# Performance work log

Measured on AMD Instinct MI355X. Metric: run time of the kernel, lower is better.

## Reference

```python
import jax, jax.numpy as jnp
import numpy as np

EMB_DIM = 2048
N_HEADS = 32
N_KV_HEADS = 8
HEAD_DIM = EMB_DIM // N_HEADS  # 64
N_REP = N_HEADS // N_KV_HEADS  # 4
B = 1
T = 2048


def setup_inputs() -> dict:
    key = jax.random.key(0)
    ks = jax.random.split(key, 7)
    x = jax.random.normal(ks[0], (B, T, EMB_DIM), dtype=jnp.float32)
    # RoPE tables, standard: cos/sin of shape (T, head_dim)
    inv_freq = 1.0 / (10000.0 ** (np.arange(0, HEAD_DIM, 2, dtype=np.float32) / HEAD_DIM))
    pos = np.arange(T, dtype=np.float32)
    ang = pos[:, None] * inv_freq[None, :]            # (T, head_dim/2)
    ang = np.concatenate([ang, ang], axis=-1)         # (T, head_dim)
    cos = jnp.asarray(np.cos(ang), dtype=jnp.float32)
    sin = jnp.asarray(np.sin(ang), dtype=jnp.float32)
    s = 0.02
    Wq = jax.random.normal(ks[1], (EMB_DIM, EMB_DIM), dtype=jnp.float32) * s
    Wk = jax.random.normal(ks[2], (N_KV_HEADS * HEAD_DIM, EMB_DIM), dtype=jnp.float32) * s
    Wv = jax.random.normal(ks[3], (N_KV_HEADS * HEAD_DIM, EMB_DIM), dtype=jnp.float32) * s
    Wo = jax.random.normal(ks[4], (EMB_DIM, EMB_DIM), dtype=jnp.float32) * s
    return {"x": x, "cos": cos, "sin": sin, "Wq": Wq, "Wk": Wk, "Wv": Wv, "Wo": Wo}


def apply_rope(t, cos, sin):
    # t: (b, h, T, d); cos/sin: (T, d)
    d = t.shape[-1]
    x1, x2 = t[..., : d // 2], t[..., d // 2:]
    rotated = jnp.concatenate([-x2, x1], axis=-1)
    return t * cos[None, None] + rotated * sin[None, None]


def reference(x, cos, sin, Wq, Wk, Wv, Wo):
    b, n_tok, _ = x.shape
    q = (x @ Wq.T).reshape(b, n_tok, N_HEADS, HEAD_DIM).transpose(0, 2, 1, 3)
    k = (x @ Wk.T).reshape(b, n_tok, N_KV_HEADS, HEAD_DIM).transpose(0, 2, 1, 3)
    v = (x @ Wv.T).reshape(b, n_tok, N_KV_HEADS, HEAD_DIM).transpose(0, 2, 1, 3)
    q = apply_rope(q, cos, sin)
    k = apply_rope(k, cos, sin)
    # repeat_interleave KV heads to n_heads
    k = jnp.repeat(k, N_REP, axis=1)
    v = jnp.repeat(v, N_REP, axis=1)
    scores = jnp.einsum("bhqd,bhkd->bhqk", q, k) / jnp.sqrt(jnp.float32(HEAD_DIM))
    causal = jnp.tril(jnp.ones((n_tok, n_tok), dtype=bool))
    scores = jnp.where(causal[None, None], scores, -jnp.inf)
    weights = jax.nn.softmax(scores, axis=-1)
    ctx = jnp.einsum("bhqk,bhkd->bhqd", weights, v)
    ctx = ctx.transpose(0, 2, 1, 3).reshape(b, n_tok, EMB_DIM)
    return ctx @ Wo.T
```

## Files before the change

kernel.cpp:

```cpp
#include <hip/hip_runtime.h>
#include <hip/hip_bf16.h>
#include <stdint.h>

#define EMB   2048
#define TOK   2048
#define NH    32
#define NKV   8
#define HD    64
#define QKVN  3072

typedef __attribute__((ext_vector_type(8))) short bf16x8;
typedef __attribute__((ext_vector_type(4))) float f32x4;
typedef __attribute__((ext_vector_type(16))) float f32x16;
typedef __attribute__((ext_vector_type(4))) unsigned int u32x4;

__device__ __forceinline__ void gld16(const void* g, void* l) {
  auto gp = reinterpret_cast<const int __attribute__((address_space(1)))*>(
      reinterpret_cast<uintptr_t>(g));
  auto lp = reinterpret_cast<int __attribute__((address_space(3)))*>(
      reinterpret_cast<uintptr_t>(l));
  __builtin_amdgcn_global_load_lds(gp, lp, 16, 0, 0);
}

__device__ __forceinline__ unsigned int cvtpk_bf16(float lo, float hi) {
  unsigned int r;
  asm("v_cvt_pk_bf16_f32 %0, %1, %2" : "=v"(r) : "v"(lo), "v"(hi));
  return r;
}
__device__ __forceinline__ void pl32swap(unsigned int &a, unsigned int &b) {
  asm volatile("v_permlane32_swap_b32 %0, %1" : "+v"(a), "+v"(b));
}
__device__ __forceinline__ float fexp2(float x) {
  float r;
  asm("v_exp_f32 %0, %1" : "=v"(r) : "v"(x));
  return r;
}

__global__ void cast_all(const float* __restrict__ x,  const float* __restrict__ wq,
                         const float* __restrict__ wk, const float* __restrict__ wv,
                         const float* __restrict__ wo,
                         __hip_bfloat16* __restrict__ xb,
                         __hip_bfloat16* __restrict__ wc,
                         __hip_bfloat16* __restrict__ wob) {
  const size_t M4 = (size_t)4 * 1024 * 1024;
  const size_t M1 = (size_t)1024 * 1024;
  size_t i = ((size_t)blockIdx.x * 256 + threadIdx.x) * 4;
  const float* src;
  __hip_bfloat16* dst;
  if (i < M4)                    { src = x  + i;                 dst = xb  + i; }
  else if (i < 2*M4)             { src = wq + (i - M4);          dst = wc  + (i - M4); }
  else if (i < 2*M4 + M1)        { src = wk + (i - 2*M4);        dst = wc  + M4 + (i - 2*M4); }
  else if (i < 2*M4 + 2*M1)      { src = wv + (i - 2*M4 - M1);   dst = wc  + M4 + M1 + (i - 2*M4 - M1); }
  else                           { src = wo + (i - 2*M4 - 2*M1); dst = wob + (i - 2*M4 - 2*M1); }
  float4 v = *reinterpret_cast<const float4*>(src);
  dst[0] = __float2bfloat16(v.x);
  dst[1] = __float2bfloat16(v.y);
  dst[2] = __float2bfloat16(v.z);
  dst[3] = __float2bfloat16(v.w);
}

template<int BN>
__global__ __launch_bounds__(512) void gemm8(const __hip_bfloat16* __restrict__ A,
                                             const __hip_bfloat16* __restrict__ B,
                                             float* __restrict__ C,
                                             int M, int N, int K) {
  constexpr int A_BYTES = 128 * 128;
  constexpr int B_BYTES = BN * 128;
  constexpr int SLOT    = A_BYTES + B_BYTES;
  constexpr int CA = 2;
  constexpr int CB = BN / 64;
  constexpr int NR = BN / 64;
  extern __shared__ char lds[];

  const int nbc = N / BN;
  const int nwg = gridDim.x;
  int bid = blockIdx.x;
  bid = (bid & 7) * (nwg >> 3) + (bid >> 3);
  const int br = bid / nbc, bc = bid % nbc;

  const int tid  = threadIdx.x;
  const int w    = tid >> 6;
  const int lane = tid & 63;
  const int wr   = w >> 2, wc = w & 3;
  const int l15  = lane & 15, lg = lane >> 4;
  const int axor = (l15 & 7) << 4;

  const __hip_bfloat16* Ag = A + (size_t)br * 128 * K;
  const __hip_bfloat16* Bg = B + (size_t)bc * BN * K;

  const int srow = lane >> 3;
  const int scol = (((lane & 7) ^ srow) << 3);

  auto stageA = [&](char* slot, int kt) {
#pragma unroll
    for (int i = 0; i < CA; ++i) {
      const int c = w * CA + i;
      gld16(Ag + (size_t)(c * 8 + srow) * K + kt + scol, slot + c * 1024);
    }
  };
  auto stageB = [&](char* slot, int kt) {
#pragma unroll
    for (int i = 0; i < CB; ++i) {
      const int c = w * CB + i;
      gld16(Bg + (size_t)(c * 8 + srow) * K + kt + scol, slot + A_BYTES + c * 1024);
    }
  };
  auto ldA = [&](const char* sa, int m, int kk) {
    return *reinterpret_cast<const bf16x8*>(
        sa + (wr * 64 + m * 16 + l15) * 128 + ((kk * 64 + lg * 16) ^ axor));
  };
  auto ldB = [&](const char* sa, int n, int kk) {
    return *reinterpret_cast<const bf16x8*>(
        sa + A_BYTES + (wc * (BN / 4) + n * 16 + l15) * 128 + ((kk * 64 + lg * 16) ^ axor));
  };

  f32x4 acc[4][NR];
#pragma unroll
  for (int m = 0; m < 4; ++m)
#pragma unroll
    for (int n = 0; n < NR; ++n) acc[m][n] = (f32x4){0.f, 0.f, 0.f, 0.f};

  const int nt = K >> 6;

  stageA(lds, 0);         stageB(lds, 0);
  stageA(lds + SLOT, 64); stageB(lds + SLOT, 64);
  if constexpr (CA + CB == 4) asm volatile("s_waitcnt vmcnt(4)" ::: "memory");
  else                        asm volatile("s_waitcnt vmcnt(5)" ::: "memory");
  __builtin_amdgcn_s_barrier();

  int slc = 0, sls = 2;
  for (int t = 0; t < nt; ++t) {
    const char* sa = lds + slc * SLOT;
    char* stg = lds + sls * SLOT;
    const bool do_stage = (t + 2) < nt;
    const int kt2 = (t + 2) << 6;

    bf16x8 afr[2][2], bfr[NR][2];
#pragma unroll
    for (int m = 0; m < 2; ++m)
#pragma unroll
      for (int kk = 0; kk < 2; ++kk) afr[m][kk] = ldA(sa, m, kk);
#pragma unroll
    for (int n = 0; n < NR; ++n)
#pragma unroll
      for (int kk = 0; kk < 2; ++kk) bfr[n][kk] = ldB(sa, n, kk);
    if (do_stage) stageA(stg, kt2);
    __builtin_amdgcn_s_barrier();
    asm volatile("s_waitcnt lgkmcnt(0)" ::: "memory");
    __builtin_amdgcn_sched_barrier(0);
    __builtin_amdgcn_s_setprio(1);
#pragma unroll
    for (int m = 0; m < 2; ++m)
#pragma unroll
      for (int n = 0; n < NR; ++n)
#pragma unroll
        for (int kk = 0; kk < 2; ++kk)
          acc[m][n] = __builtin_amdgcn_mfma_f32_16x16x32_bf16(afr[m][kk], bfr[n][kk],
                                                              acc[m][n], 0, 0, 0);
    __builtin_amdgcn_s_setprio(0);
    __builtin_amdgcn_s_barrier();

#pragma unroll
    for (int m = 0; m < 2; ++m)
#pragma unroll
      for (int kk = 0; kk < 2; ++kk) afr[m][kk] = ldA(sa, 2 + m, kk);
    if (do_stage) stageB(stg, kt2);
    __builtin_amdgcn_s_barrier();
    asm volatile("s_waitcnt lgkmcnt(0)" ::: "memory");
    __builtin_amdgcn_sched_barrier(0);
    __builtin_amdgcn_s_setprio(1);
#pragma unroll
    for (int m = 0; m < 2; ++m)
#pragma unroll
      for (int n = 0; n < NR; ++n)
#pragma unroll
        for (int kk = 0; kk < 2; ++kk)
          acc[2 + m][n] = __builtin_amdgcn_mfma_f32_16x16x32_bf16(afr[m][kk], bfr[n][kk],
                                                                  acc[2 + m][n], 0, 0, 0);
    __builtin_amdgcn_s_setprio(0);
    if (t < nt - 2) {
      if constexpr (CA + CB == 4) asm volatile("s_waitcnt vmcnt(4)" ::: "memory");
      else                        asm volatile("s_waitcnt vmcnt(5)" ::: "memory");
    } else {
      asm volatile("s_waitcnt vmcnt(0)" ::: "memory");
    }
    __builtin_amdgcn_s_barrier();

    slc = (slc == 2) ? 0 : slc + 1;
    sls = (sls == 2) ? 0 : sls + 1;
  }

  const int row0 = br * 128 + wr * 64;
  const int col0 = bc * BN + wc * (BN / 4);
#pragma unroll
  for (int m = 0; m < 4; ++m)
#pragma unroll
    for (int n = 0; n < NR; ++n)
#pragma unroll
      for (int r = 0; r < 4; ++r)
        C[(size_t)(row0 + m * 16 + lg * 4 + r) * N + col0 + n * 16 + l15] = acc[m][n][r];
}

#define QSCALE 0.1803368801111243f

__device__ __forceinline__ size_t kq_idx(int tile_row, int t, int d) {
  return ((size_t)tile_row) * 2048 +
         ((((d >> 4) * 64) + (((d >> 3) & 1) * 32) + (t & 31)) << 3) + (d & 7);
}

__global__ void rope_cast(const float* __restrict__ qkv,
                          const float* __restrict__ cosT, const float* __restrict__ sinT,
                          __hip_bfloat16* __restrict__ Qf,
                          __hip_bfloat16* __restrict__ Kf,
                          __hip_bfloat16* __restrict__ Vf) {
  const int QP = TOK * NH * (HD / 2);
  const int KP = TOK * NKV * (HD / 2);
  int idx = blockIdx.x * 256 + threadIdx.x;
  if (idx < QP) {
    int d = idx & 31, h = (idx >> 5) & 31, t = idx >> 10;
    const float* row = qkv + (size_t)t * QKVN + h * 64;
    float x1 = row[d], x2 = row[d + 32];
    float o1 = (x1 * cosT[t * 64 + d]      - x2 * sinT[t * 64 + d])      * QSCALE;
    float o2 = (x2 * cosT[t * 64 + d + 32] + x1 * sinT[t * 64 + d + 32]) * QSCALE;
    const int tile_row = h * 64 + (t >> 5);
    Qf[kq_idx(tile_row, t, d)]      = __float2bfloat16(o1);
    Qf[kq_idx(tile_row, t, d + 32)] = __float2bfloat16(o2);
  } else if (idx < QP + KP) {
    int j = idx - QP;
    int d = j & 31, hk = (j >> 5) & 7, t = j >> 8;
    const float* row = qkv + (size_t)t * QKVN + 2048 + hk * 64;
    float x1 = row[d], x2 = row[d + 32];
    float o1 = x1 * cosT[t * 64 + d]      - x2 * sinT[t * 64 + d];
    float o2 = x2 * cosT[t * 64 + d + 32] + x1 * sinT[t * 64 + d + 32];
    const int tile_row = hk * 64 + (t >> 5);
    Kf[kq_idx(tile_row, t, d)]      = __float2bfloat16(o1);
    Kf[kq_idx(tile_row, t, d + 32)] = __float2bfloat16(o2);
  } else {
    int vj = idx - QP - KP;
    int d = vj & 63, t = (vj >> 6) & (TOK - 1), hk = vj >> 17;
    float v = qkv[(size_t)t * QKVN + 2560 + hk * 64 + d];
    const size_t tb = ((size_t)hk * 64 + (t >> 5)) * 2048;
    const int c = (((t >> 4) & 1) * 128) + ((d >> 5) * 64) + (((t >> 3) & 1) * 32) + (d & 31);
    Vf[tb + (c << 3) + (t & 7)] = __float2bfloat16(v);
  }
}

#define MBIAS 10.0f

struct KVb { bf16x8 k0, k1, k2, k3, v00, v01, v10, v11; };

__device__ __forceinline__ void load_kv(KVb& b, const __hip_bfloat16* Kt,
                                        const __hip_bfloat16* Vt, int tile,
                                        int lane) {
  const __hip_bfloat16* Kp = Kt + (size_t)tile * 2048 + lane * 8;
  b.k0 = *reinterpret_cast<const bf16x8*>(Kp);
  b.k1 = *reinterpret_cast<const bf16x8*>(Kp + 512);
  b.k2 = *reinterpret_cast<const bf16x8*>(Kp + 1024);
  b.k3 = *reinterpret_cast<const bf16x8*>(Kp + 1536);
  const __hip_bfloat16* Vp = Vt + (size_t)tile * 2048 + lane * 8;
  b.v00 = *reinterpret_cast<const bf16x8*>(Vp);
  b.v10 = *reinterpret_cast<const bf16x8*>(Vp + 512);
  b.v01 = *reinterpret_cast<const bf16x8*>(Vp + 1024);
  b.v11 = *reinterpret_cast<const bf16x8*>(Vp + 1536);
}

__device__ __forceinline__ void compute_tile(const KVb& b, bool diag,
                                             const bf16x8 (&qf)[4],
                                             const f32x16& minit,
                                             int l31, int hi,
                                             float& mb, float& l,
                                             f32x16& oa0, f32x16& oa1) {
  __builtin_amdgcn_s_setprio(1);
  f32x16 st = __builtin_amdgcn_mfma_f32_32x32x16_bf16(b.k0, qf[0], minit, 0, 0, 0);
  st = __builtin_amdgcn_mfma_f32_32x32x16_bf16(b.k1, qf[1], st, 0, 0, 0);
  st = __builtin_amdgcn_mfma_f32_32x32x16_bf16(b.k2, qf[2], st, 0, 0, 0);
  st = __builtin_amdgcn_mfma_f32_32x32x16_bf16(b.k3, qf[3], st, 0, 0, 0);
  __builtin_amdgcn_s_setprio(0);

  float s[16];
#pragma unroll
  for (int r = 0; r < 16; ++r) s[r] = st[r];
  if (diag) {
#pragma unroll
    for (int r = 0; r < 16; ++r) {
      const int crow = (r & 3) + 8 * (r >> 2) + 4 * hi;
      s[r] = (crow <= l31) ? s[r] : -1e30f;
    }
  }
  float a0 = fmaxf(fmaxf(s[0], s[1]),  s[2]);
  float a1 = fmaxf(fmaxf(s[3], s[4]),  s[5]);
  float a2 = fmaxf(fmaxf(s[6], s[7]),  s[8]);
  float a3 = fmaxf(fmaxf(s[9], s[10]), s[11]);
  float a4 = fmaxf(fmaxf(s[12], s[13]), s[14]);
  float rmax = fmaxf(fmaxf(fmaxf(fmaxf(a0, a1), a2), fmaxf(a3, a4)), s[15]);
  rmax = fmaxf(rmax, __shfl_xor(rmax, 32));

  if (!__all(rmax <= mb + 8.0f)) {
    const float mnew = fmaxf(mb, rmax);
    const float resc = fexp2(mb - mnew);
    l *= resc;
#pragma unroll
    for (int r = 0; r < 16; ++r) { oa0[r] *= resc; oa1[r] *= resc; }
    mb = mnew;
  }

  float p[16];
  if (mb == 0.0f) {
#pragma unroll
    for (int r = 0; r < 16; ++r) p[r] = fexp2(s[r]);
  } else {
#pragma unroll
    for (int r = 0; r < 16; ++r) p[r] = fexp2(s[r] - mb);
  }
  float u0 = (p[0] + p[1]) + (p[2] + p[3]);
  float u1 = (p[4] + p[5]) + (p[6] + p[7]);
  float u2 = (p[8] + p[9]) + (p[10] + p[11]);
  float u3 = (p[12] + p[13]) + (p[14] + p[15]);
  float rsum = (u0 + u1) + (u2 + u3);
  rsum += __shfl_xor(rsum, 32);
  l += rsum;

  unsigned int wpk[8];
#pragma unroll
  for (int j = 0; j < 8; ++j) wpk[j] = cvtpk_bf16(p[2 * j], p[2 * j + 1]);

  __builtin_amdgcn_s_setprio(1);
  {
    unsigned int x0 = wpk[0], y0 = wpk[2];  pl32swap(x0, y0);
    unsigned int x1 = wpk[1], y1 = wpk[3];  pl32swap(x1, y1);
    u32x4 pw; pw[0] = x0; pw[1] = x1; pw[2] = y0; pw[3] = y1;
    bf16x8 pf = *reinterpret_cast<bf16x8*>(&pw);
    oa0 = __builtin_amdgcn_mfma_f32_32x32x16_bf16(b.v00, pf, oa0, 0, 0, 0);
    oa1 = __builtin_amdgcn_mfma_f32_32x32x16_bf16(b.v10, pf, oa1, 0, 0, 0);
  }
  {
    unsigned int x0 = wpk[4], y0 = wpk[6];  pl32swap(x0, y0);
    unsigned int x1 = wpk[5], y1 = wpk[7];  pl32swap(x1, y1);
    u32x4 pw; pw[0] = x0; pw[1] = x1; pw[2] = y0; pw[3] = y1;
    bf16x8 pf = *reinterpret_cast<bf16x8*>(&pw);
    oa0 = __builtin_amdgcn_mfma_f32_32x32x16_bf16(b.v01, pf, oa0, 0, 0, 0);
    oa1 = __builtin_amdgcn_mfma_f32_32x32x16_bf16(b.v11, pf, oa1, 0, 0, 0);
  }
  __builtin_amdgcn_s_setprio(0);
}

__global__ __launch_bounds__(128) void attn6(const __hip_bfloat16* __restrict__ Qf,
                                             const __hip_bfloat16* __restrict__ Kf,
                                             const __hip_bfloat16* __restrict__ Vf,
                                             __hip_bfloat16* __restrict__ ctx) {
  const int h     = blockIdx.x & 31;
  const int strip = 63 - (blockIdx.x >> 5);
  const int hk    = h >> 2;
  const int tid   = threadIdx.x;
  const int w     = tid >> 6;
  const int lane  = tid & 63;
  const int l31   = lane & 31, hi = lane >> 5;
  const int q0    = strip * 32;
  const int nt    = strip + 1;

  __shared__ unsigned int part_u[2][32][33];
  __shared__ float mlb[2][2][32];

  const __hip_bfloat16* Kt = Kf + (size_t)hk * 64 * 2048;
  const __hip_bfloat16* Vt = Vf + (size_t)hk * 64 * 2048;

  const __hip_bfloat16* Qp = Qf + ((size_t)h * 64 + strip) * 2048 + lane * 8;
  bf16x8 qf[4];
#pragma unroll
  for (int ks = 0; ks < 4; ++ks)
    qf[ks] = *reinterpret_cast<const bf16x8*>(Qp + ks * 512);

  f32x16 minit;
#pragma unroll
  for (int r = 0; r < 16; ++r) minit[r] = -MBIAS;

  f32x16 oa0, oa1;
#pragma unroll
  for (int r = 0; r < 16; ++r) { oa0[r] = 0.f; oa1[r] = 0.f; }
  float mb = 0.f, l = 0.f;

  if (w < nt) {
    KVb A, B;
    load_kv(A, Kt, Vt, w, lane);
    int t = w;
    for (;;) {
      int nx = t + 2;
      if (nx < nt) load_kv(B, Kt, Vt, nx, lane);
      compute_tile(A, t == nt - 1, qf, minit, l31, hi, mb, l, oa0, oa1);
      t = nx;
      if (t >= nt) break;
      nx = t + 2;
      if (nx < nt) load_kv(A, Kt, Vt, nx, lane);
      compute_tile(B, t == nt - 1, qf, minit, l31, hi, mb, l, oa0, oa1);
      t = nx;
      if (t >= nt) break;
    }
  }

#pragma unroll
  for (int r = 0; r < 16; ++r) {
    const int d0 = (r & 3) + 8 * (r >> 2) + 4 * hi;
    part_u[w][d0][l31] = cvtpk_bf16(oa0[r], oa1[r]);
  }
  if (hi == 0) { mlb[w][0][l31] = mb; mlb[w][1][l31] = l; }
  __syncthreads();

  const int d  = tid & 63;
  const int qg = tid >> 6;
#pragma unroll
  for (int qq = 0; qq < 16; ++qq) {
    const int q = qg * 16 + qq;
    const float m0 = mlb[0][0][q], m1 = mlb[1][0][q];
    const float M = fmaxf(m0, m1);
    const float s0 = fexp2(m0 - M), s1 = fexp2(m1 - M);
    const float L = mlb[0][1][q] * s0 + mlb[1][1][q] * s1;
    const unsigned int u0 = part_u[0][d & 31][q];
    const unsigned int u1 = part_u[1][d & 31][q];
    const unsigned int w0 = (d < 32) ? (u0 << 16) : (u0 & 0xffff0000u);
    const unsigned int w1 = (d < 32) ? (u1 << 16) : (u1 & 0xffff0000u);
    const float p0 = __uint_as_float(w0), p1 = __uint_as_float(w1);
    ctx[(size_t)(q0 + q) * EMB + h * HD + d] = __float2bfloat16((p0 * s0 + p1 * s1) / L);
  }
}

extern "C" void kernel_launch(void* const* d_in, const int* in_sizes, int n_in,
                              void* d_out, int out_size, void* d_ws, size_t ws_size,
                              hipStream_t stream) {
  const float* x    = (const float*)d_in[0];
  const float* cosT = (const float*)d_in[1];
  const float* sinT = (const float*)d_in[2];
  const float* Wq   = (const float*)d_in[3];
  const float* Wk   = (const float*)d_in[4];
  const float* Wv   = (const float*)d_in[5];
  const float* Wo   = (const float*)d_in[6];
  float* out = (float*)d_out;

  const size_t M4 = (size_t)4 * 1024 * 1024;
  const size_t M1 = (size_t)1024 * 1024;

  char* ws = (char*)d_ws;
  __hip_bfloat16* xb   = (__hip_bfloat16*)ws;
  __hip_bfloat16* Wc   = xb + M4;
  __hip_bfloat16* Wob  = Wc + (size_t)6 * M1;
  float*          qkv  = (float*)(Wob + M4);
  __hip_bfloat16* Qf   = (__hip_bfloat16*)(qkv + (size_t)TOK * QKVN);
  __hip_bfloat16* Kf   = Qf + (size_t)NH * TOK * HD;
  __hip_bfloat16* Vf   = Kf + (size_t)NKV * TOK * HD;
  __hip_bfloat16* ctxb = Vf + (size_t)NKV * HD * TOK;

  constexpr int SLOT192 = 128 * 128 + 192 * 128;
  constexpr int SLOT128 = 128 * 128 + 128 * 128;
  hipFuncSetAttribute(reinterpret_cast<const void*>(&gemm8<192>),
                      hipFuncAttributeMaxDynamicSharedMemorySize, 3 * SLOT192);
  hipFuncSetAttribute(reinterpret_cast<const void*>(&gemm8<128>),
                      hipFuncAttributeMaxDynamicSharedMemorySize, 3 * SLOT128);

  cast_all<<<14336, 256, 0, stream>>>(x, Wq, Wk, Wv, Wo, xb, Wc, Wob);

  gemm8<192><<<256, 512, 3 * SLOT192, stream>>>(xb, Wc, qkv, TOK, QKVN, EMB);

  rope_cast<<<14336, 256, 0, stream>>>(qkv, cosT, sinT, Qf, Kf, Vf);

  attn6<<<64 * 32, 128, 0, stream>>>(Qf, Kf, Vf, ctxb);

  gemm8<128><<<256, 512, 3 * SLOT128, stream>>>(ctxb, Wob, out, TOK, EMB, EMB);
}
```

Measured before the change: 122.9 us.

## Split attention KV range into fixed-size chunks with separate merge kernel

The old kernel gave each 32-query strip a 2-wave block that split KV tiles between its two waves. The new attention kernel splits each strip into work units of at most 16 KV tiles (1 to 4 units depending on strip length), one wave per block. Each unit writes bf16 partial outputs plus max/sum stats into the qkv scratch buffer, and a new merge kernel combines them. This aims to balance load across the causal triangle and raise the number of independent blocks. In exchange it adds an extra launch, a global round trip for partial results, and one wave per block instead of two.

```diff
diff --git a/kernel.cpp b/kernel.cpp
--- a/kernel.cpp
+++ b/kernel.cpp
@@ -246,6 +246,7 @@
 }
 
 #define MBIAS 10.0f
+#define UPH   160
 
 struct KVb { bf16x8 k0, k1, k2, k3, v00, v01, v10, v11; };
 
@@ -344,27 +345,31 @@
   __builtin_amdgcn_s_setprio(0);
 }
 
-__global__ __launch_bounds__(128) void attn6(const __hip_bfloat16* __restrict__ Qf,
-                                             const __hip_bfloat16* __restrict__ Kf,
-                                             const __hip_bfloat16* __restrict__ Vf,
-                                             __hip_bfloat16* __restrict__ ctx) {
-  const int h     = blockIdx.x & 31;
-  const int strip = 63 - (blockIdx.x >> 5);
-  const int hk    = h >> 2;
-  const int tid   = threadIdx.x;
-  const int w     = tid >> 6;
-  const int lane  = tid & 63;
-  const int l31   = lane & 31, hi = lane >> 5;
-  const int q0    = strip * 32;
-  const int nt    = strip + 1;
-
-  __shared__ unsigned int part_u[2][32][33];
-  __shared__ float mlb[2][2][32];
+__global__ __launch_bounds__(64) void attn7(const __hip_bfloat16* __restrict__ Qf,
+                                            const __hip_bfloat16* __restrict__ Kf,
+                                            const __hip_bfloat16* __restrict__ Vf,
+                                            unsigned int* __restrict__ po,
+                                            float* __restrict__ pml) {
+  const int h  = blockIdx.x & 31;
+  const int fu = (UPH - 1) - (blockIdx.x >> 5);
+  int s, c;
+  if (fu < 16)      { s = fu; c = 0; }
+  else if (fu < 48) { int q = fu - 16; s = 16 + (q >> 1); c = q & 1; }
+  else if (fu < 96) { int q = fu - 48; int d3 = q / 3; s = 32 + d3; c = q - 3 * d3; }
+  else              { int q = fu - 96; s = 48 + (q >> 2); c = q & 3; }
+  const int hk   = h >> 2;
+  const int lane = threadIdx.x;
+  const int l31  = lane & 31, hi = lane >> 5;
+  const int nt   = s + 1;
+  const int t0   = c * 16;
+  const int t1   = (t0 + 16 < nt) ? t0 + 16 : nt;
+
+  __shared__ unsigned int T[32][33];
 
   const __hip_bfloat16* Kt = Kf + (size_t)hk * 64 * 2048;
   const __hip_bfloat16* Vt = Vf + (size_t)hk * 64 * 2048;
 
-  const __hip_bfloat16* Qp = Qf + ((size_t)h * 64 + strip) * 2048 + lane * 8;
+  const __hip_bfloat16* Qp = Qf + ((size_t)h * 64 + s) * 2048 + lane * 8;
   bf16x8 qf[4];
 #pragma unroll
   for (int ks = 0; ks < 4; ++ks)
@@ -379,47 +384,71 @@
   for (int r = 0; r < 16; ++r) { oa0[r] = 0.f; oa1[r] = 0.f; }
   float mb = 0.f, l = 0.f;
 
-  if (w < nt) {
-    KVb A, B;
-    load_kv(A, Kt, Vt, w, lane);
-    int t = w;
-    for (;;) {
-      int nx = t + 2;
-      if (nx < nt) load_kv(B, Kt, Vt, nx, lane);
-      compute_tile(A, t == nt - 1, qf, minit, l31, hi, mb, l, oa0, oa1);
-      t = nx;
-      if (t >= nt) break;
-      nx = t + 2;
-      if (nx < nt) load_kv(A, Kt, Vt, nx, lane);
-      compute_tile(B, t == nt - 1, qf, minit, l31, hi, mb, l, oa0, oa1);
-      t = nx;
-      if (t >= nt) break;
-    }
-  }
-
+  KVb A, B;
+  load_kv(A, Kt, Vt, t0, lane);
+  int t = t0;
+  for (;;) {
+    int nx = t + 1;
+    if (nx < t1) load_kv(B, Kt, Vt, nx, lane);
+    compute_tile(A, t == nt - 1, qf, minit, l31, hi, mb, l, oa0, oa1);
+    t = nx;
+    if (t >= t1) break;
+    nx = t + 1;
+    if (nx < t1) load_kv(A, Kt, Vt, nx, lane);
+    compute_tile(B, t == nt - 1, qf, minit, l31, hi, mb, l, oa0, oa1);
+    t = nx;
+    if (t >= t1) break;
+  }
+
+  const int slot = h * UPH + fu;
 #pragma unroll
   for (int r = 0; r < 16; ++r) {
     const int d0 = (r & 3) + 8 * (r >> 2) + 4 * hi;
-    part_u[w][d0][l31] = cvtpk_bf16(oa0[r], oa1[r]);
-  }
-  if (hi == 0) { mlb[w][0][l31] = mb; mlb[w][1][l31] = l; }
-  __syncthreads();
-
-  const int d  = tid & 63;
-  const int qg = tid >> 6;
-#pragma unroll
-  for (int qq = 0; qq < 16; ++qq) {
-    const int q = qg * 16 + qq;
-    const float m0 = mlb[0][0][q], m1 = mlb[1][0][q];
-    const float M = fmaxf(m0, m1);
-    const float s0 = fexp2(m0 - M), s1 = fexp2(m1 - M);
-    const float L = mlb[0][1][q] * s0 + mlb[1][1][q] * s1;
-    const unsigned int u0 = part_u[0][d & 31][q];
-    const unsigned int u1 = part_u[1][d & 31][q];
-    const unsigned int w0 = (d < 32) ? (u0 << 16) : (u0 & 0xffff0000u);
-    const unsigned int w1 = (d < 32) ? (u1 << 16) : (u1 & 0xffff0000u);
-    const float p0 = __uint_as_float(w0), p1 = __uint_as_float(w1);
-    ctx[(size_t)(q0 + q) * EMB + h * HD + d] = __float2bfloat16((p0 * s0 + p1 * s1) / L);
+    T[d0][l31] = cvtpk_bf16(oa0[r], oa1[r]);
+  }
+  unsigned int* slotp = po + (size_t)slot * 1024;
+#pragma unroll
+  for (int k = 0; k < 16; ++k) {
+    const int idx = k * 64 + lane;
+    slotp[idx] = T[idx & 31][idx >> 5];
+  }
+  if (hi == 0) {
+    pml[slot * 64 + l31]      = mb;
+    pml[slot * 64 + 32 + l31] = l;
+  }
+}
+
+__global__ __launch_bounds__(64) void attn_merge(const unsigned int* __restrict__ po,
+                                                 const float* __restrict__ pml,
+                                                 __hip_bfloat16* __restrict__ ctx) {
+  const int h = blockIdx.x & 31;
+  const int s = blockIdx.x >> 5;
+  const int d = threadIdx.x;
+  const int nu  = (s >> 4) + 1;
+  const int seg = s >> 4;
+  const int base = (seg == 0) ? s
+                 : (seg == 1) ? 16 + (s - 16) * 2
+                 : (seg == 2) ? 48 + (s - 32) * 3
+                 :              96 + (s - 48) * 4;
+  const int slot0 = h * UPH + base;
+
+  for (int q = 0; q < 32; ++q) {
+    float mm[4], ll[4];
+    float M = -1e30f;
+    for (int u = 0; u < nu; ++u) {
+      mm[u] = pml[(slot0 + u) * 64 + q];
+      ll[u] = pml[(slot0 + u) * 64 + 32 + q];
+      M = fmaxf(M, mm[u]);
+    }
+    float L = 0.f, val = 0.f;
+    for (int u = 0; u < nu; ++u) {
+      const float sc = fexp2(mm[u] - M);
+      L += ll[u] * sc;
+      const unsigned int pu = po[(size_t)(slot0 + u) * 1024 + q * 32 + (d & 31)];
+      const unsigned int wv = (d < 32) ? (pu << 16) : (pu & 0xffff0000u);
+      val += __uint_as_float(wv) * sc;
+    }
+    ctx[(size_t)(s * 32 + q) * EMB + h * HD + d] = __float2bfloat16(val / L);
   }
 }
 
@@ -448,6 +477,9 @@
   __hip_bfloat16* Vf   = Kf + (size_t)NKV * TOK * HD;
   __hip_bfloat16* ctxb = Vf + (size_t)NKV * HD * TOK;
 
+  unsigned int* po  = (unsigned int*)qkv;
+  float*        pml = (float*)(po + (size_t)32 * UPH * 1024);
+
   constexpr int SLOT192 = 128 * 128 + 192 * 128;
   constexpr int SLOT128 = 128 * 128 + 128 * 128;
   hipFuncSetAttribute(reinterpret_cast<const void*>(&gemm8<192>),
@@ -461,7 +493,8 @@
 
   rope_cast<<<14336, 256, 0, stream>>>(qkv, cosT, sinT, Qf, Kf, Vf);
 
-  attn6<<<64 * 32, 128, 0, stream>>>(Qf, Kf, Vf, ctxb);
+  attn7<<<32 * UPH, 64, 0, stream>>>(Qf, Kf, Vf, po, pml);
+  attn_merge<<<32 * 64, 64, 0, stream>>>(po, pml, ctxb);
 
   gemm8<128><<<256, 512, 3 * SLOT128, stream>>>(ctxb, Wob, out, TOK, EMB, EMB);
 }
```

Result: slower. 172.8 us (+40.6%).

## Process two query strips per attention block with four waves sharing KV tiles

Applied to the files above, without the earlier changes.

The attention kernel now gives each 256-thread block two adjacent 32-row query strips of one head, and spreads the KV tiles across four waves instead of two. Each loaded KV tile is applied to both query strips, so global K/V traffic per query row is roughly halved and more waves overlap per block. Partial outputs from the four waves are merged through shared memory with a four-way softmax rescale. The costs are more registers per wave (two Q sets and four accumulators), half as many blocks, a larger shared-memory footprint, and idle waves on the shortest strips.

```diff
diff --git a/kernel.cpp b/kernel.cpp
--- a/kernel.cpp
+++ b/kernel.cpp
@@ -344,82 +344,107 @@
   __builtin_amdgcn_s_setprio(0);
 }
 
-__global__ __launch_bounds__(128) void attn6(const __hip_bfloat16* __restrict__ Qf,
+__global__ __launch_bounds__(256) void attn9(const __hip_bfloat16* __restrict__ Qf,
                                              const __hip_bfloat16* __restrict__ Kf,
                                              const __hip_bfloat16* __restrict__ Vf,
                                              __hip_bfloat16* __restrict__ ctx) {
-  const int h     = blockIdx.x & 31;
-  const int strip = 63 - (blockIdx.x >> 5);
-  const int hk    = h >> 2;
-  const int tid   = threadIdx.x;
-  const int w     = tid >> 6;
-  const int lane  = tid & 63;
-  const int l31   = lane & 31, hi = lane >> 5;
-  const int q0    = strip * 32;
-  const int nt    = strip + 1;
-
-  __shared__ unsigned int part_u[2][32][33];
-  __shared__ float mlb[2][2][32];
+  const int idx = blockIdx.x;
+  const int hk  = idx & 7;
+  const int hq  = (idx >> 3) & 3;
+  const int p   = 31 - (idx >> 5);
+  const int h   = hk * 4 + hq;
+  const int tid = threadIdx.x;
+  const int w   = tid >> 6;
+  const int lane = tid & 63;
+  const int l31  = lane & 31, hi = lane >> 5;
+  const int sA = 2 * p, sB = 2 * p + 1;
+  const int NT = 2 * p + 2;
+
+  __shared__ unsigned int part_u[4][2][32][33];
+  __shared__ float mlb[4][2][2][32];
 
   const __hip_bfloat16* Kt = Kf + (size_t)hk * 64 * 2048;
   const __hip_bfloat16* Vt = Vf + (size_t)hk * 64 * 2048;
 
-  const __hip_bfloat16* Qp = Qf + ((size_t)h * 64 + strip) * 2048 + lane * 8;
-  bf16x8 qf[4];
-#pragma unroll
-  for (int ks = 0; ks < 4; ++ks)
-    qf[ks] = *reinterpret_cast<const bf16x8*>(Qp + ks * 512);
+  bf16x8 qfA[4], qfB[4];
+  {
+    const __hip_bfloat16* QpA = Qf + ((size_t)h * 64 + sA) * 2048 + lane * 8;
+    const __hip_bfloat16* QpB = Qf + ((size_t)h * 64 + sB) * 2048 + lane * 8;
+#pragma unroll
+    for (int ks = 0; ks < 4; ++ks) {
+      qfA[ks] = *reinterpret_cast<const bf16x8*>(QpA + ks * 512);
+      qfB[ks] = *reinterpret_cast<const bf16x8*>(QpB + ks * 512);
+    }
+  }
 
   f32x16 minit;
 #pragma unroll
   for (int r = 0; r < 16; ++r) minit[r] = -MBIAS;
 
-  f32x16 oa0, oa1;
-#pragma unroll
-  for (int r = 0; r < 16; ++r) { oa0[r] = 0.f; oa1[r] = 0.f; }
-  float mb = 0.f, l = 0.f;
-
-  if (w < nt) {
-    KVb A, B;
-    load_kv(A, Kt, Vt, w, lane);
+  f32x16 oaA0, oaA1, oaB0, oaB1;
+#pragma unroll
+  for (int r = 0; r < 16; ++r) { oaA0[r] = 0.f; oaA1[r] = 0.f; oaB0[r] = 0.f; oaB1[r] = 0.f; }
+  float mbA = 0.f, lA = 0.f, mbB = 0.f, lB = 0.f;
+
+  if (w < NT) {
+    KVb b0, b1;
+    load_kv(b0, Kt, Vt, w, lane);
     int t = w;
     for (;;) {
-      int nx = t + 2;
-      if (nx < nt) load_kv(B, Kt, Vt, nx, lane);
-      compute_tile(A, t == nt - 1, qf, minit, l31, hi, mb, l, oa0, oa1);
+      int nx = t + 4;
+      if (nx < NT) load_kv(b1, Kt, Vt, nx, lane);
+      if (t <= sA) compute_tile(b0, t == sA, qfA, minit, l31, hi, mbA, lA, oaA0, oaA1);
+      compute_tile(b0, t == sB, qfB, minit, l31, hi, mbB, lB, oaB0, oaB1);
       t = nx;
-      if (t >= nt) break;
-      nx = t + 2;
-      if (nx < nt) load_kv(A, Kt, Vt, nx, lane);
-      compute_tile(B, t == nt - 1, qf, minit, l31, hi, mb, l, oa0, oa1);
+      if (t >= NT) break;
+      nx = t + 4;
+      if (nx < NT) load_kv(b0, Kt, Vt, nx, lane);
+      if (t <= sA) compute_tile(b1, t == sA, qfA, minit, l31, hi, mbA, lA, oaA0, oaA1);
+      compute_tile(b1, t == sB, qfB, minit, l31, hi, mbB, lB, oaB0, oaB1);
       t = nx;
-      if (t >= nt) break;
+      if (t >= NT) break;
     }
   }
 
 #pragma unroll
   for (int r = 0; r < 16; ++r) {
     const int d0 = (r & 3) + 8 * (r >> 2) + 4 * hi;
-    part_u[w][d0][l31] = cvtpk_bf16(oa0[r], oa1[r]);
-  }
-  if (hi == 0) { mlb[w][0][l31] = mb; mlb[w][1][l31] = l; }
+    part_u[w][0][d0][l31] = cvtpk_bf16(oaA0[r], oaA1[r]);
+    part_u[w][1][d0][l31] = cvtpk_bf16(oaB0[r], oaB1[r]);
+  }
+  if (hi == 0) {
+    mlb[w][0][0][l31] = mbA; mlb[w][0][1][l31] = lA;
+    mlb[w][1][0][l31] = mbB; mlb[w][1][1][l31] = lB;
+  }
   __syncthreads();
 
   const int d  = tid & 63;
   const int qg = tid >> 6;
 #pragma unroll
   for (int qq = 0; qq < 16; ++qq) {
-    const int q = qg * 16 + qq;
-    const float m0 = mlb[0][0][q], m1 = mlb[1][0][q];
-    const float M = fmaxf(m0, m1);
+    const int Xq = qg * 16 + qq;
+    const int X  = Xq >> 5;
+    const int q  = Xq & 31;
+    const float m0 = mlb[0][X][0][q], m1 = mlb[1][X][0][q];
+    const float m2 = mlb[2][X][0][q], m3 = mlb[3][X][0][q];
+    const float M = fmaxf(fmaxf(m0, m1), fmaxf(m2, m3));
     const float s0 = fexp2(m0 - M), s1 = fexp2(m1 - M);
-    const float L = mlb[0][1][q] * s0 + mlb[1][1][q] * s1;
-    const unsigned int u0 = part_u[0][d & 31][q];
-    const unsigned int u1 = part_u[1][d & 31][q];
-    const unsigned int w0 = (d < 32) ? (u0 << 16) : (u0 & 0xffff0000u);
-    const unsigned int w1 = (d < 32) ? (u1 << 16) : (u1 & 0xffff0000u);
-    const float p0 = __uint_as_float(w0), p1 = __uint_as_float(w1);
-    ctx[(size_t)(q0 + q) * EMB + h * HD + d] = __float2bfloat16((p0 * s0 + p1 * s1) / L);
+    const float s2 = fexp2(m2 - M), s3 = fexp2(m3 - M);
+    const float L = mlb[0][X][1][q] * s0 + mlb[1][X][1][q] * s1 +
+                    mlb[2][X][1][q] * s2 + mlb[3][X][1][q] * s3;
+    const unsigned int u0 = part_u[0][X][d & 31][q];
+    const unsigned int u1 = part_u[1][X][d & 31][q];
+    const unsigned int u2 = part_u[2][X][d & 31][q];
+    const unsigned int u3 = part_u[3][X][d & 31][q];
+    const unsigned int msk = (d < 32) ? 0u : 0xffff0000u;
+    const int sh = (d < 32) ? 16 : 0;
+    const float p0 = __uint_as_float((u0 << sh) & (msk | 0xffff0000u));
+    const float p1 = __uint_as_float((u1 << sh) & (msk | 0xffff0000u));
+    const float p2 = __uint_as_float((u2 << sh) & (msk | 0xffff0000u));
+    const float p3 = __uint_as_float((u3 << sh) & (msk | 0xffff0000u));
+    const float val = p0 * s0 + p1 * s1 + p2 * s2 + p3 * s3;
+    const int row = 64 * p + X * 32 + q;
+    ctx[(size_t)row * EMB + h * HD + d] = __float2bfloat16(val / L);
   }
 }
 
@@ -461,7 +486,7 @@
 
   rope_cast<<<14336, 256, 0, stream>>>(qkv, cosT, sinT, Qf, Kf, Vf);
 
-  attn6<<<64 * 32, 128, 0, stream>>>(Qf, Kf, Vf, ctxb);
+  attn9<<<1024, 256, 0, stream>>>(Qf, Kf, Vf, ctxb);
 
   gemm8<128><<<256, 512, 3 * SLOT128, stream>>>(ctxb, Wob, out, TOK, EMB, EMB);
 }
```

Result: slower. 144.0 us (+17.1%).
